# Kernel tuning notes

Hardware: AMD Instinct MI355X
Metric: run time of the kernel (lower is better)

Reference implementation:

```python
import jax, jax.numpy as jnp
import numpy as np

N_NODES = 50000
N_EDGES = 640000
N_REL = 8
IN_DIM = 128
HID_DIM = 128
OUT_DIM = 64


def setup_inputs() -> dict:
    key = jax.random.key(0)
    ks = jax.random.split(key, 8)
    features = jax.random.normal(ks[0], (N_NODES, IN_DIM), dtype=jnp.float32)
    src = jax.random.randint(ks[1], (N_EDGES,), 0, N_NODES, dtype=jnp.int32)
    dst = jax.random.randint(ks[2], (N_EDGES,), 0, N_NODES, dtype=jnp.int32)
    edge_types = jax.random.randint(ks[3], (N_EDGES,), 0, N_REL, dtype=jnp.int32)
    s1 = 1.0 / np.sqrt(IN_DIM)
    s2 = 1.0 / np.sqrt(HID_DIM)
    W1 = jax.random.normal(ks[4], (N_REL, IN_DIM, HID_DIM), dtype=jnp.float32) * s1
    W1_self = jax.random.normal(ks[5], (IN_DIM, HID_DIM), dtype=jnp.float32) * s1
    b1 = jnp.zeros((HID_DIM,), dtype=jnp.float32)
    W2 = jax.random.normal(ks[6], (N_REL, HID_DIM, OUT_DIM), dtype=jnp.float32) * s2
    W2_self = jax.random.normal(ks[7], (HID_DIM, OUT_DIM), dtype=jnp.float32) * s2
    b2 = jnp.zeros((OUT_DIM,), dtype=jnp.float32)
    return {"features": features, "src": src, "dst": dst, "edge_types": edge_types,
            "W1": W1, "W1_self": W1_self, "b1": b1,
            "W2": W2, "W2_self": W2_self, "b2": b2}


def _rel_graph_conv(h, src, dst, edge_types, W, W_self, b):
    # Precompute relation-specific transforms for all nodes: [R, N, Dout]
    rel = jnp.einsum('nd,rdo->rno', h, W)
    # Gather per-edge message W[etype(e)] @ h[src(e)]: [E, Dout]
    msg = rel[edge_types, src]
    # Scatter-sum to destination nodes
    agg = jax.ops.segment_sum(msg, dst, num_segments=h.shape[0])
    # Self-loop + bias (DGL RelGraphConv defaults: self_loop=True, bias=True)
    return agg + h @ W_self + b


def reference(features, src, dst, edge_types, W1, W1_self, b1, W2, W2_self, b2):
    h = jax.nn.relu(_rel_graph_conv(features, src, dst, edge_types, W1, W1_self, b1))
    logits = _rel_graph_conv(h, src, dst, edge_types, W2, W2_self, b2)
    return logits
```

## Files before the change

### kernel.cpp

```cpp
#include <hip/hip_runtime.h>
#include <hip/hip_bf16.h>
#include <stdint.h>

#define NN 50000
#define NE 640000
#define NR 8
#define NK (NR * NN)
#define NB2 ((NK + 1023) / 1024)

typedef short bf16x8 __attribute__((ext_vector_type(8)));
typedef float f32x4  __attribute__((ext_vector_type(4)));

__device__ __forceinline__ unsigned short f2bf(float f) {
    union { float f; unsigned u; } v; v.f = f;
    unsigned r = v.u + 0x7FFF + ((v.u >> 16) & 1);
    return (unsigned short)(r >> 16);
}

__global__ void hist2_kernel(const int* __restrict__ dst, const int* __restrict__ et,
                             int* __restrict__ counts) {
    int e = blockIdx.x * 256 + threadIdx.x;
    if (e < NE) atomicAdd(&counts[et[e] * NN + dst[e]], 1);
}

__global__ __launch_bounds__(1024) void blocksum_kernel(const int* __restrict__ counts,
                                                        int* __restrict__ bsum, int n) {
    __shared__ int ws[16];
    int i = blockIdx.x * 1024 + threadIdx.x;
    int v = (i < n) ? counts[i] : 0;
    #pragma unroll
    for (int d = 32; d > 0; d >>= 1) v += __shfl_down(v, d, 64);
    int wid = threadIdx.x >> 6, lane = threadIdx.x & 63;
    if (lane == 0) ws[wid] = v;
    __syncthreads();
    if (threadIdx.x < 16) {
        int s = ws[threadIdx.x];
        #pragma unroll
        for (int d = 8; d > 0; d >>= 1) s += __shfl_down(s, d, 16);
        if (threadIdx.x == 0) bsum[blockIdx.x] = s;
    }
}

__global__ __launch_bounds__(512) void scanbase_kernel(const int* __restrict__ bsum,
                                                       int* __restrict__ base,
                                                       int* __restrict__ total, int nb) {
    __shared__ int ws[8];
    int t = threadIdx.x, lane = t & 63, wid = t >> 6;
    int v = (t < nb) ? bsum[t] : 0;
    int incl = v;
    #pragma unroll
    for (int d = 1; d < 64; d <<= 1) {
        int nv = __shfl_up(incl, d, 64);
        if (lane >= d) incl += nv;
    }
    if (lane == 63) ws[wid] = incl;
    __syncthreads();
    if (t < 8) {
        int s = ws[t], si = s;
        #pragma unroll
        for (int d = 1; d < 8; d <<= 1) {
            int nv = __shfl_up(si, d, 8);
            if (t >= d) si += nv;
        }
        ws[t] = si - s;
    }
    __syncthreads();
    int excl = ws[wid] + incl - v;
    if (t < nb) base[t] = excl;
    if (t == 511) total[0] = ws[7] + incl;
}

__global__ __launch_bounds__(1024) void scanlocal_kernel(const int* __restrict__ counts,
                                                         const int* __restrict__ base,
                                                         int* __restrict__ offsets,
                                                         int* __restrict__ cursor, int n) {
    __shared__ int ws[16];
    __shared__ int wbase[16];
    int t = threadIdx.x;
    int i = blockIdx.x * 1024 + t;
    int v = (i < n) ? counts[i] : 0;
    int lane = t & 63, wid = t >> 6;
    int incl = v;
    #pragma unroll
    for (int d = 1; d < 64; d <<= 1) {
        int nv = __shfl_up(incl, d, 64);
        if (lane >= d) incl += nv;
    }
    if (lane == 63) ws[wid] = incl;
    __syncthreads();
    if (t < 16) {
        int s = ws[t], si = s;
        #pragma unroll
        for (int d = 1; d < 16; d <<= 1) {
            int nv = __shfl_up(si, d, 16);
            if (t >= d) si += nv;
        }
        wbase[t] = si - s;
    }
    __syncthreads();
    if (i < n) {
        int excl = base[blockIdx.x] + wbase[wid] + incl - v;
        offsets[i] = excl;
        cursor[i]  = excl;
    }
}

__global__ void fill2_kernel(const int* __restrict__ src, const int* __restrict__ dst,
                             const int* __restrict__ et, int* __restrict__ cursor,
                             int* __restrict__ esrc) {
    int e = blockIdx.x * 256 + threadIdx.x;
    if (e < NE) {
        int pos = atomicAdd(&cursor[et[e] * NN + dst[e]], 1);
        esrc[pos] = src[e];
    }
}

__global__ void cvt_bf16_kernel(const float* __restrict__ in, unsigned short* __restrict__ outp,
                                int n8) {
    int i = blockIdx.x * 256 + threadIdx.x;
    if (i >= n8) return;
    const float4* pp = (const float4*)in + (size_t)i * 2;
    float4 a = pp[0], b = pp[1];
    uint4 o;
    o.x = (unsigned)f2bf(a.x) | ((unsigned)f2bf(a.y) << 16);
    o.y = (unsigned)f2bf(a.z) | ((unsigned)f2bf(a.w) << 16);
    o.z = (unsigned)f2bf(b.x) | ((unsigned)f2bf(b.y) << 16);
    o.w = (unsigned)f2bf(b.z) | ((unsigned)f2bf(b.w) << 16);
    ((uint4*)outp)[i] = o;
}

template<int DOUTV>
__global__ void prepW_kernel(const float* __restrict__ W, const float* __restrict__ Wself,
                             unsigned short* __restrict__ WT) {
    int idx = blockIdx.x * 256 + threadIdx.x;
    if (idx >= 9 * DOUTV * 128) return;
    int k = idx & 127;
    int c = idx >> 7;
    int r = c / DOUTV;
    int o = c - r * DOUTV;
    float v = (r < 8) ? W[((size_t)r * 128 + k) * DOUTV + o]
                      : Wself[(size_t)k * DOUTV + o];
    WT[idx] = f2bf(v);
}

template<int NOUT, bool RELU, bool OUTBF16>
__global__ __launch_bounds__(256) void fused_layer(
        const unsigned short* __restrict__ A,
        const unsigned short* __restrict__ WT,
        const float* __restrict__ bias,
        const int* __restrict__ off2,
        const int* __restrict__ esrc,
        void* __restrict__ outp, int M) {
    constexpr int RB = 32;
    constexpr int CW = NOUT / 4;
    constexpr int NJ = CW / 16;
    __shared__ unsigned short Asw[RB * 128];

    const int t = threadIdx.x;
    const int n0 = blockIdx.x * RB;
    const int bm = (M - n0 < RB) ? (M - n0) : RB;
    const int lane = t & 63;
    const int w = t >> 6;
    const int r15 = lane & 15;
    const int q = lane >> 4;

    const int key = t >> 3;
    const int sub = t & 7;
    const int kk = n0 + key;
    const bool kv = (kk < M);

    f32x4 acc[2][NJ] = {};

    auto do_mfma = [&](int rr) {
        #pragma unroll
        for (int ks = 0; ks < 4; ks++) {
            int c = (ks * 4 + q) ^ r15;
            bf16x8 af[2];
            #pragma unroll
            for (int i = 0; i < 2; i++)
                af[i] = *(const bf16x8*)((const char*)Asw + (i * 16 + r15) * 256 + (c << 4));
            #pragma unroll
            for (int j = 0; j < NJ; j++) {
                bf16x8 bf = *(const bf16x8*)(WT +
                    ((size_t)(rr * NOUT + w * CW + j * 16 + r15) << 7) + ks * 32 + q * 8);
                #pragma unroll
                for (int i = 0; i < 2; i++)
                    acc[i][j] = __builtin_amdgcn_mfma_f32_16x16x32_bf16(af[i], bf, acc[i][j], 0, 0, 0);
            }
        }
    };

    int e0 = kv ? off2[kk] : 0;
    int e1 = kv ? off2[kk + 1] : 0;

    #pragma unroll
    for (int kc = 0; kc < 2; kc++) {
        int g = t + kc * 256;
        int row = g >> 4, c = g & 15;
        uint4 v = make_uint4(0, 0, 0, 0);
        if (row < bm) v = *(const uint4*)(A + ((size_t)(n0 + row) << 7) + c * 8);
        *(uint4*)((char*)Asw + row * 256 + ((c ^ (row & 15)) << 4)) = v;
    }
    __syncthreads();
    do_mfma(8);

    for (int r = 0; r < 8; r++) {
        int e0n = 0, e1n = 0;
        if (r < 7 && kv) {
            e0n = off2[(r + 1) * NN + kk];
            e1n = off2[(r + 1) * NN + kk + 1];
        }

        float a[16];
        #pragma unroll
        for (int i = 0; i < 16; i++) a[i] = 0.f;
        for (int e = e0; e < e1; ++e) {
            int s = esrc[e];
            const uint4* rp = (const uint4*)((const unsigned*)A + ((size_t)s << 6) + sub * 8);
            #pragma unroll
            for (int u4 = 0; u4 < 2; ++u4) {
                uint4 v = rp[u4];
                unsigned uu[4] = {v.x, v.y, v.z, v.w};
                #pragma unroll
                for (int j = 0; j < 4; ++j) {
                    a[u4 * 8 + j * 2 + 0] += __uint_as_float(uu[j] << 16);
                    a[u4 * 8 + j * 2 + 1] += __uint_as_float(uu[j] & 0xffff0000u);
                }
            }
        }
        __syncthreads();

        #pragma unroll
        for (int c4 = 0; c4 < 2; ++c4) {
            uint4 pv;
            pv.x = (unsigned)f2bf(a[c4 * 8 + 0]) | ((unsigned)f2bf(a[c4 * 8 + 1]) << 16);
            pv.y = (unsigned)f2bf(a[c4 * 8 + 2]) | ((unsigned)f2bf(a[c4 * 8 + 3]) << 16);
            pv.z = (unsigned)f2bf(a[c4 * 8 + 4]) | ((unsigned)f2bf(a[c4 * 8 + 5]) << 16);
            pv.w = (unsigned)f2bf(a[c4 * 8 + 6]) | ((unsigned)f2bf(a[c4 * 8 + 7]) << 16);
            int c = sub * 2 + c4;
            *(uint4*)((char*)Asw + key * 256 + ((c ^ (key & 15)) << 4)) = pv;
        }
        __syncthreads();

        do_mfma(r);
        e0 = e0n; e1 = e1n;
    }

    #pragma unroll
    for (int j = 0; j < NJ; j++) {
        int col = w * CW + j * 16 + r15;
        float bv = bias[col];
        #pragma unroll
        for (int i = 0; i < 2; i++) {
            #pragma unroll
            for (int reg = 0; reg < 4; reg++) {
                int m = n0 + i * 16 + q * 4 + reg;
                if (m < M) {
                    float v = acc[i][j][reg] + bv;
                    if (RELU) v = fmaxf(v, 0.f);
                    if (OUTBF16)
                        ((unsigned short*)outp)[(size_t)m * NOUT + col] = f2bf(v);
                    else
                        ((float*)outp)[(size_t)m * NOUT + col] = v;
                }
            }
        }
    }
}

extern "C" void kernel_launch(void* const* d_in, const int* in_sizes, int n_in,
                              void* d_out, int out_size, void* d_ws, size_t ws_size,
                              hipStream_t stream) {
    const float* X   = (const float*)d_in[0];
    const int*   src = (const int*)d_in[1];
    const int*   dst = (const int*)d_in[2];
    const int*   et  = (const int*)d_in[3];
    const float* W1  = (const float*)d_in[4];
    const float* W1s = (const float*)d_in[5];
    const float* b1  = (const float*)d_in[6];
    const float* W2  = (const float*)d_in[7];
    const float* W2s = (const float*)d_in[8];
    const float* b2  = (const float*)d_in[9];
    float* out = (float*)d_out;

    char* p = (char*)d_ws;
    unsigned short* Xbf = (unsigned short*)p; p += (size_t)NN * 128 * 2;
    unsigned short* hbf = (unsigned short*)p; p += (size_t)NN * 128 * 2;
    unsigned short* W1T = (unsigned short*)p; p += (size_t)9 * 128 * 128 * 2;
    unsigned short* W2T = (unsigned short*)p; p += (size_t)9 * 64 * 128 * 2;
    int* counts2 = (int*)p; p += (size_t)NK * 4;
    int* off2    = (int*)p; p += (size_t)(NK + 4) * 4;
    int* cursor2 = (int*)p; p += (size_t)NK * 4;
    int* esrc    = (int*)p; p += (size_t)NE * 4;
    int* bsum    = (int*)p; p += 512 * 4;
    int* bbase   = (int*)p; p += 512 * 4;

    hipMemsetAsync(counts2, 0, (size_t)NK * sizeof(int), stream);
    hist2_kernel<<<(NE + 255) / 256, 256, 0, stream>>>(dst, et, counts2);
    blocksum_kernel<<<NB2, 1024, 0, stream>>>(counts2, bsum, NK);
    scanbase_kernel<<<1, 512, 0, stream>>>(bsum, bbase, &off2[NK], NB2);
    scanlocal_kernel<<<NB2, 1024, 0, stream>>>(counts2, bbase, off2, cursor2, NK);
    fill2_kernel<<<(NE + 255) / 256, 256, 0, stream>>>(src, dst, et, cursor2, esrc);

    cvt_bf16_kernel<<<(NN * 128 / 8 + 255) / 256, 256, 0, stream>>>(X, Xbf, NN * 128 / 8);
    prepW_kernel<128><<<(9 * 128 * 128 + 255) / 256, 256, 0, stream>>>(W1, W1s, W1T);
    prepW_kernel<64><<<(9 * 64 * 128 + 255) / 256, 256, 0, stream>>>(W2, W2s, W2T);

    const int nblk = (NN + 31) / 32;

    fused_layer<128, true, true><<<nblk, 256, 0, stream>>>(
        Xbf, W1T, b1, off2, esrc, hbf, NN);
    fused_layer<64, false, false><<<nblk, 256, 0, stream>>>(
        hbf, W2T, b2, off2, esrc, out, NN);
}
```

Before: 332.7 us.

## Merge preprocessing into one cooperative kernel and enlarge fused-layer row tiles

The memset, histogram, three scan kernels, CSR fill, feature conversion and weight transposes are folded into a single cooperative kernel of 391 blocks that uses grid.sync between phases. This removes nine separate launches and their gaps. The fused layer kernel now handles 64 rows per block instead of 32, with 4 threads per node each gathering 32 features, so each weight fragment load is reused across more MFMA tiles. The cost is higher register pressure from doubled accumulators, fewer blocks in flight, and serialization at the grid barriers.

Result: slower. 534.0 us (+60.5%).

```diff
diff --git a/kernel.cpp b/kernel.cpp
--- a/kernel.cpp
+++ b/kernel.cpp
@@ -1,12 +1,15 @@
 #include <hip/hip_runtime.h>
 #include <hip/hip_bf16.h>
+#include <hip/hip_cooperative_groups.h>
 #include <stdint.h>
+
+namespace cg = cooperative_groups;
 
 #define NN 50000
 #define NE 640000
 #define NR 8
 #define NK (NR * NN)
-#define NB2 ((NK + 1023) / 1024)
+#define NPB 391
 
 typedef short bf16x8 __attribute__((ext_vector_type(8)));
 typedef float f32x4  __attribute__((ext_vector_type(4)));
@@ -17,36 +20,58 @@
     return (unsigned short)(r >> 16);
 }
 
-__global__ void hist2_kernel(const int* __restrict__ dst, const int* __restrict__ et,
-                             int* __restrict__ counts) {
-    int e = blockIdx.x * 256 + threadIdx.x;
-    if (e < NE) atomicAdd(&counts[et[e] * NN + dst[e]], 1);
-}
-
-__global__ __launch_bounds__(1024) void blocksum_kernel(const int* __restrict__ counts,
-                                                        int* __restrict__ bsum, int n) {
+__global__ __launch_bounds__(1024, 8) void prep_all(
+        const float* __restrict__ X,
+        const float* __restrict__ W1, const float* __restrict__ W1s,
+        const float* __restrict__ W2, const float* __restrict__ W2s,
+        const int* __restrict__ src, const int* __restrict__ dst,
+        const int* __restrict__ et,
+        unsigned short* __restrict__ Xbf,
+        unsigned short* __restrict__ W1T, unsigned short* __restrict__ W2T,
+        int* __restrict__ counts, int* __restrict__ off2,
+        int* __restrict__ cursor, int* __restrict__ esrc,
+        int* __restrict__ bsum, int* __restrict__ bbase) {
+    cg::grid_group grid = cg::this_grid();
+    const int t = threadIdx.x, b = blockIdx.x;
+    const int gid = b * 1024 + t;
+    const int gsz = gridDim.x * 1024;
+    const int lane = t & 63, wid = t >> 6;
     __shared__ int ws[16];
-    int i = blockIdx.x * 1024 + threadIdx.x;
-    int v = (i < n) ? counts[i] : 0;
-    #pragma unroll
-    for (int d = 32; d > 0; d >>= 1) v += __shfl_down(v, d, 64);
-    int wid = threadIdx.x >> 6, lane = threadIdx.x & 63;
-    if (lane == 0) ws[wid] = v;
-    __syncthreads();
-    if (threadIdx.x < 16) {
-        int s = ws[threadIdx.x];
-        #pragma unroll
-        for (int d = 8; d > 0; d >>= 1) s += __shfl_down(s, d, 16);
-        if (threadIdx.x == 0) bsum[blockIdx.x] = s;
-    }
-}
-
-__global__ __launch_bounds__(512) void scanbase_kernel(const int* __restrict__ bsum,
-                                                       int* __restrict__ base,
-                                                       int* __restrict__ total, int nb) {
-    __shared__ int ws[8];
-    int t = threadIdx.x, lane = t & 63, wid = t >> 6;
-    int v = (t < nb) ? bsum[t] : 0;
+    __shared__ int wbase[16];
+
+    for (int i = gid; i < NK; i += gsz) counts[i] = 0;
+    for (int i = gid; i < NN * 16; i += gsz) {
+        const float4* pp = (const float4*)X + (size_t)i * 2;
+        float4 a = pp[0], c = pp[1];
+        uint4 o;
+        o.x = (unsigned)f2bf(a.x) | ((unsigned)f2bf(a.y) << 16);
+        o.y = (unsigned)f2bf(a.z) | ((unsigned)f2bf(a.w) << 16);
+        o.z = (unsigned)f2bf(c.x) | ((unsigned)f2bf(c.y) << 16);
+        o.w = (unsigned)f2bf(c.z) | ((unsigned)f2bf(c.w) << 16);
+        ((uint4*)Xbf)[i] = o;
+    }
+    for (int i = gid; i < 9 * 128 * 128; i += gsz) {
+        int k = i & 127, c = i >> 7;
+        int r = c >> 7, o = c & 127;
+        float v = (r < 8) ? W1[((size_t)r * 128 + k) * 128 + o]
+                          : W1s[(size_t)k * 128 + o];
+        W1T[i] = f2bf(v);
+    }
+    for (int i = gid; i < 9 * 64 * 128; i += gsz) {
+        int k = i & 127, c = i >> 7;
+        int r = c >> 6, o = c & 63;
+        float v = (r < 8) ? W2[((size_t)r * 128 + k) * 64 + o]
+                          : W2s[(size_t)k * 64 + o];
+        W2T[i] = f2bf(v);
+    }
+    grid.sync();
+
+    for (int e = gid; e < NE; e += gsz)
+        atomicAdd(&counts[et[e] * NN + dst[e]], 1);
+    grid.sync();
+
+    int i2 = b * 1024 + t;
+    int v = (i2 < NK) ? counts[i2] : 0;
     int incl = v;
     #pragma unroll
     for (int d = 1; d < 64; d <<= 1) {
@@ -55,39 +80,6 @@
     }
     if (lane == 63) ws[wid] = incl;
     __syncthreads();
-    if (t < 8) {
-        int s = ws[t], si = s;
-        #pragma unroll
-        for (int d = 1; d < 8; d <<= 1) {
-            int nv = __shfl_up(si, d, 8);
-            if (t >= d) si += nv;
-        }
-        ws[t] = si - s;
-    }
-    __syncthreads();
-    int excl = ws[wid] + incl - v;
-    if (t < nb) base[t] = excl;
-    if (t == 511) total[0] = ws[7] + incl;
-}
-
-__global__ __launch_bounds__(1024) void scanlocal_kernel(const int* __restrict__ counts,
-                                                         const int* __restrict__ base,
-                                                         int* __restrict__ offsets,
-                                                         int* __restrict__ cursor, int n) {
-    __shared__ int ws[16];
-    __shared__ int wbase[16];
-    int t = threadIdx.x;
-    int i = blockIdx.x * 1024 + t;
-    int v = (i < n) ? counts[i] : 0;
-    int lane = t & 63, wid = t >> 6;
-    int incl = v;
-    #pragma unroll
-    for (int d = 1; d < 64; d <<= 1) {
-        int nv = __shfl_up(incl, d, 64);
-        if (lane >= d) incl += nv;
-    }
-    if (lane == 63) ws[wid] = incl;
-    __syncthreads();
     if (t < 16) {
         int s = ws[t], si = s;
         #pragma unroll
@@ -98,49 +90,47 @@
         wbase[t] = si - s;
     }
     __syncthreads();
-    if (i < n) {
-        int excl = base[blockIdx.x] + wbase[wid] + incl - v;
-        offsets[i] = excl;
-        cursor[i]  = excl;
-    }
-}
-
-__global__ void fill2_kernel(const int* __restrict__ src, const int* __restrict__ dst,
-                             const int* __restrict__ et, int* __restrict__ cursor,
-                             int* __restrict__ esrc) {
-    int e = blockIdx.x * 256 + threadIdx.x;
-    if (e < NE) {
+    int local_excl = wbase[wid] + incl - v;
+    if (t == 0) bsum[b] = wbase[15] + ws[15];
+    grid.sync();
+
+    if (b == 0) {
+        int nb = gridDim.x;
+        int vv = (t < nb) ? bsum[t] : 0;
+        int inc2 = vv;
+        #pragma unroll
+        for (int d = 1; d < 64; d <<= 1) {
+            int nv = __shfl_up(inc2, d, 64);
+            if (lane >= d) inc2 += nv;
+        }
+        if (lane == 63) ws[wid] = inc2;
+        __syncthreads();
+        if (t < 16) {
+            int s = ws[t], si = s;
+            #pragma unroll
+            for (int d = 1; d < 16; d <<= 1) {
+                int nv = __shfl_up(si, d, 16);
+                if (t >= d) si += nv;
+            }
+            wbase[t] = si - s;
+        }
+        __syncthreads();
+        if (t < nb) bbase[t] = wbase[wid] + inc2 - vv;
+    }
+    grid.sync();
+
+    if (i2 < NK) {
+        int e2 = bbase[b] + local_excl;
+        off2[i2] = e2;
+        cursor[i2] = e2;
+    }
+    if (gid == 0) off2[NK] = NE;
+    grid.sync();
+
+    for (int e = gid; e < NE; e += gsz) {
         int pos = atomicAdd(&cursor[et[e] * NN + dst[e]], 1);
         esrc[pos] = src[e];
     }
-}
-
-__global__ void cvt_bf16_kernel(const float* __restrict__ in, unsigned short* __restrict__ outp,
-                                int n8) {
-    int i = blockIdx.x * 256 + threadIdx.x;
-    if (i >= n8) return;
-    const float4* pp = (const float4*)in + (size_t)i * 2;
-    float4 a = pp[0], b = pp[1];
-    uint4 o;
-    o.x = (unsigned)f2bf(a.x) | ((unsigned)f2bf(a.y) << 16);
-    o.y = (unsigned)f2bf(a.z) | ((unsigned)f2bf(a.w) << 16);
-    o.z = (unsigned)f2bf(b.x) | ((unsigned)f2bf(b.y) << 16);
-    o.w = (unsigned)f2bf(b.z) | ((unsigned)f2bf(b.w) << 16);
-    ((uint4*)outp)[i] = o;
-}
-
-template<int DOUTV>
-__global__ void prepW_kernel(const float* __restrict__ W, const float* __restrict__ Wself,
-                             unsigned short* __restrict__ WT) {
-    int idx = blockIdx.x * 256 + threadIdx.x;
-    if (idx >= 9 * DOUTV * 128) return;
-    int k = idx & 127;
-    int c = idx >> 7;
-    int r = c / DOUTV;
-    int o = c - r * DOUTV;
-    float v = (r < 8) ? W[((size_t)r * 128 + k) * DOUTV + o]
-                      : Wself[(size_t)k * DOUTV + o];
-    WT[idx] = f2bf(v);
 }
 
 template<int NOUT, bool RELU, bool OUTBF16>
@@ -151,40 +141,39 @@
         const int* __restrict__ off2,
         const int* __restrict__ esrc,
         void* __restrict__ outp, int M) {
-    constexpr int RB = 32;
     constexpr int CW = NOUT / 4;
     constexpr int NJ = CW / 16;
-    __shared__ unsigned short Asw[RB * 128];
+    __shared__ unsigned short Asw[64 * 128];
 
     const int t = threadIdx.x;
-    const int n0 = blockIdx.x * RB;
-    const int bm = (M - n0 < RB) ? (M - n0) : RB;
+    const int n0 = blockIdx.x * 64;
+    const int bm = (M - n0 < 64) ? (M - n0) : 64;
     const int lane = t & 63;
     const int w = t >> 6;
     const int r15 = lane & 15;
     const int q = lane >> 4;
 
-    const int key = t >> 3;
-    const int sub = t & 7;
+    const int key = t >> 2;
+    const int sub = t & 3;
     const int kk = n0 + key;
     const bool kv = (kk < M);
 
-    f32x4 acc[2][NJ] = {};
+    f32x4 acc[4][NJ] = {};
 
     auto do_mfma = [&](int rr) {
         #pragma unroll
         for (int ks = 0; ks < 4; ks++) {
             int c = (ks * 4 + q) ^ r15;
-            bf16x8 af[2];
-            #pragma unroll
-            for (int i = 0; i < 2; i++)
+            bf16x8 af[4];
+            #pragma unroll
+            for (int i = 0; i < 4; i++)
                 af[i] = *(const bf16x8*)((const char*)Asw + (i * 16 + r15) * 256 + (c << 4));
             #pragma unroll
             for (int j = 0; j < NJ; j++) {
                 bf16x8 bf = *(const bf16x8*)(WT +
                     ((size_t)(rr * NOUT + w * CW + j * 16 + r15) << 7) + ks * 32 + q * 8);
                 #pragma unroll
-                for (int i = 0; i < 2; i++)
+                for (int i = 0; i < 4; i++)
                     acc[i][j] = __builtin_amdgcn_mfma_f32_16x16x32_bf16(af[i], bf, acc[i][j], 0, 0, 0);
             }
         }
@@ -194,7 +183,7 @@
     int e1 = kv ? off2[kk + 1] : 0;
 
     #pragma unroll
-    for (int kc = 0; kc < 2; kc++) {
+    for (int kc = 0; kc < 4; kc++) {
         int g = t + kc * 256;
         int row = g >> 4, c = g & 15;
         uint4 v = make_uint4(0, 0, 0, 0);
@@ -211,14 +200,14 @@
             e1n = off2[(r + 1) * NN + kk + 1];
         }
 
-        float a[16];
-        #pragma unroll
-        for (int i = 0; i < 16; i++) a[i] = 0.f;
+        float a[32];
+        #pragma unroll
+        for (int i = 0; i < 32; i++) a[i] = 0.f;
         for (int e = e0; e < e1; ++e) {
             int s = esrc[e];
-            const uint4* rp = (const uint4*)((const unsigned*)A + ((size_t)s << 6) + sub * 8);
-            #pragma unroll
-            for (int u4 = 0; u4 < 2; ++u4) {
+            const uint4* rp = (const uint4*)((const unsigned*)A + ((size_t)s << 6) + sub * 16);
+            #pragma unroll
+            for (int u4 = 0; u4 < 4; ++u4) {
                 uint4 v = rp[u4];
                 unsigned uu[4] = {v.x, v.y, v.z, v.w};
                 #pragma unroll
@@ -231,13 +220,13 @@
         __syncthreads();
 
         #pragma unroll
-        for (int c4 = 0; c4 < 2; ++c4) {
+        for (int c4 = 0; c4 < 4; ++c4) {
             uint4 pv;
             pv.x = (unsigned)f2bf(a[c4 * 8 + 0]) | ((unsigned)f2bf(a[c4 * 8 + 1]) << 16);
             pv.y = (unsigned)f2bf(a[c4 * 8 + 2]) | ((unsigned)f2bf(a[c4 * 8 + 3]) << 16);
             pv.z = (unsigned)f2bf(a[c4 * 8 + 4]) | ((unsigned)f2bf(a[c4 * 8 + 5]) << 16);
             pv.w = (unsigned)f2bf(a[c4 * 8 + 6]) | ((unsigned)f2bf(a[c4 * 8 + 7]) << 16);
-            int c = sub * 2 + c4;
+            int c = sub * 4 + c4;
             *(uint4*)((char*)Asw + key * 256 + ((c ^ (key & 15)) << 4)) = pv;
         }
         __syncthreads();
@@ -251,7 +240,7 @@
         int col = w * CW + j * 16 + r15;
         float bv = bias[col];
         #pragma unroll
-        for (int i = 0; i < 2; i++) {
+        for (int i = 0; i < 4; i++) {
             #pragma unroll
             for (int reg = 0; reg < 4; reg++) {
                 int m = n0 + i * 16 + q * 4 + reg;
@@ -295,18 +284,17 @@
     int* bsum    = (int*)p; p += 512 * 4;
     int* bbase   = (int*)p; p += 512 * 4;
 
-    hipMemsetAsync(counts2, 0, (size_t)NK * sizeof(int), stream);
-    hist2_kernel<<<(NE + 255) / 256, 256, 0, stream>>>(dst, et, counts2);
-    blocksum_kernel<<<NB2, 1024, 0, stream>>>(counts2, bsum, NK);
-    scanbase_kernel<<<1, 512, 0, stream>>>(bsum, bbase, &off2[NK], NB2);
-    scanlocal_kernel<<<NB2, 1024, 0, stream>>>(counts2, bbase, off2, cursor2, NK);
-    fill2_kernel<<<(NE + 255) / 256, 256, 0, stream>>>(src, dst, et, cursor2, esrc);
-
-    cvt_bf16_kernel<<<(NN * 128 / 8 + 255) / 256, 256, 0, stream>>>(X, Xbf, NN * 128 / 8);
-    prepW_kernel<128><<<(9 * 128 * 128 + 255) / 256, 256, 0, stream>>>(W1, W1s, W1T);
-    prepW_kernel<64><<<(9 * 64 * 128 + 255) / 256, 256, 0, stream>>>(W2, W2s, W2T);
-
-    const int nblk = (NN + 31) / 32;
+    void* args[] = {
+        (void*)&X, (void*)&W1, (void*)&W1s, (void*)&W2, (void*)&W2s,
+        (void*)&src, (void*)&dst, (void*)&et,
+        (void*)&Xbf, (void*)&W1T, (void*)&W2T,
+        (void*)&counts2, (void*)&off2, (void*)&cursor2, (void*)&esrc,
+        (void*)&bsum, (void*)&bbase
+    };
+    hipLaunchCooperativeKernel((void*)prep_all, dim3(NPB), dim3(1024),
+                               args, 0, stream);
+
+    const int nblk = (NN + 63) / 64;
 
     fused_layer<128, true, true><<<nblk, 256, 0, stream>>>(
         Xbf, W1T, b1, off2, esrc, hbf, NN);
```
